# Kernel optimization log

Measured on AMD Instinct MI355X. Metric: run time of the kernel, lower is better.

The kernel has to match this reference:

```python
import jax, jax.numpy as jnp
import numpy as np


def _sqdist(X1, X2):
    # squared euclidean distance matrix, matches torch.cdist(...,p=2)**2
    d2 = (jnp.sum(X1 * X1, -1)[:, None] + jnp.sum(X2 * X2, -1)[None, :]
          - 2.0 * (X1 @ X2.T))
    return jnp.maximum(d2, 0.0)


def setup_inputs() -> dict:
    key = jax.random.key(0)
    k1, k2, k3, k4, k5, k6 = jax.random.split(key, 6)
    n, m, d, C = 1024, 2048, 4, 64
    X_train = jax.random.normal(k1, (n, d), dtype=jnp.float32)
    y_train = jax.random.normal(k2, (n,), dtype=jnp.float32)
    X_test = jax.random.normal(k3, (m, d), dtype=jnp.float32)
    # positive params within the priors' supports
    lengthscale = jax.random.uniform(k4, (C,), minval=0.1, maxval=3.0, dtype=jnp.float32)
    variance = jax.random.uniform(k5, (C,), minval=0.1, maxval=3.0, dtype=jnp.float32)
    noise = jax.random.uniform(k6, (C,), minval=0.01, maxval=0.5, dtype=jnp.float32)
    return {"X_train": X_train, "y_train": y_train, "X_test": X_test,
            "lengthscale": lengthscale, "variance": variance, "noise": noise}


def reference(X_train, y_train, X_test, lengthscale, variance, noise):
    n = X_train.shape[0]
    ls2 = (lengthscale ** 2)[:, None, None]          # [C,1,1]
    var = variance[:, None, None]                     # [C,1,1]
    d2_tr = _sqdist(X_train, X_train)                 # [n,n]
    d2_te = _sqdist(X_test, X_train)                  # [m,n]
    K_train = var * jnp.exp(-0.5 * d2_tr[None] / ls2)   # [C,n,n]
    K_test = var * jnp.exp(-0.5 * d2_te[None] / ls2)    # [C,m,n]
    K_noisy = K_train + noise[:, None, None] * jnp.eye(n, dtype=K_train.dtype)
    L = jnp.linalg.cholesky(K_noisy)                  # batched [C,n,n]

    def per_chain(Lc, Ktc):
        solve = jax.scipy.linalg.solve_triangular
        z = solve(Lc, y_train, lower=True)            # [n]
        alpha = solve(Lc, z, lower=True, trans=1)     # [n]
        pred_mean = Ktc @ alpha                       # [m]
        v = solve(Lc, Ktc.T, lower=True)              # [n,m]
        pred_var = jnp.sum(v * v, axis=0)             # [m]
        return pred_mean, pred_var

    means, vars_ = jax.vmap(per_chain)(L, K_test)     # [C,m] each
    return means.mean(axis=0), vars_.mean(axis=0)
```

## Files before the change

### kernel.cpp

```cpp
#include <hip/hip_runtime.h>
#include <hip/hip_fp16.h>
#include <math.h>

#define N 1024
#define M 2048
#define C 64
#define NB 128
#define TB 8
#define NBLK 36
#define PL ((size_t)NBLK*NB*NB)

typedef __attribute__((ext_vector_type(8))) short bf16x8;
typedef __attribute__((ext_vector_type(8))) _Float16 f16x8;
typedef __attribute__((ext_vector_type(4))) float f32x4;

__device__ __forceinline__ size_t pblk(int ib, int jt){
    return ((size_t)((ib*(ib+1))/2 + jt))*((size_t)NB*NB);
}

#define TT(r,c) T[(r)][(((c)+(r)) & 127)]


__device__ __forceinline__ float sqdist4(const float4 a, const float4 b){
    float dx=a.x-b.x, dy=a.y-b.y, dz=a.z-b.z, dw=a.w-b.w;
    return dx*dx+dy*dy+dz*dz+dw*dw;
}

__device__ __forceinline__ void split4(float x0, float x1, float x2, float x3,
                                       uint2& hi, uint2& lo){
    unsigned b0=__float_as_uint(x0), b1=__float_as_uint(x1),
             b2=__float_as_uint(x2), b3=__float_as_uint(x3);
    unsigned h0=b0&0xFFFF0000u, h1=b1&0xFFFF0000u, h2=b2&0xFFFF0000u, h3=b3&0xFFFF0000u;
    hi.x = (h0>>16)|h1;  hi.y = (h2>>16)|h3;
    float l0=x0-__uint_as_float(h0), l1=x1-__uint_as_float(h1),
          l2=x2-__uint_as_float(h2), l3=x3-__uint_as_float(h3);
    lo.x = (__float_as_uint(l0)>>16) | (__float_as_uint(l1)&0xFFFF0000u);
    lo.y = (__float_as_uint(l2)>>16) | (__float_as_uint(l3)&0xFFFF0000u);
}

__device__ void chol_invert_lds(float T[NB][NB], int tid){
    for (int j = 0; j < NB; j++){
        float d = TT(j,j);
        float inv = 1.0f / sqrtf(d);
        for (int i = j+1+tid; i < NB; i += 256) TT(i,j) *= inv;
        if (tid == 0) TT(j,j) = d * inv;
        __syncthreads();
        int i = j+1 + (tid >> 1);
        if (i < NB){
            float lij = TT(i,j);
            for (int k = j+1+(tid&1); k <= i; k += 2)
                TT(i,k) -= lij * TT(k,j);
        }
        __syncthreads();
    }
    for (int i = 0; i < NB; i++){
        float inv_ii = 1.0f / TT(i,i);
        int j = tid & 127, hi = tid >> 7;
        float S = 0.0f;
        if (j < i){
            for (int k = i-1-hi; k >= j; k -= 2)
                S += TT(i,k) * TT(k,j);
        }
        if (hi && j < i) TT(j,i) = S;
        __syncthreads();
        if (!hi){
            if (j < i)      TT(i,j) = -inv_ii * (S + TT(j,i));
            else if (j == i) TT(i,i) = inv_ii;
        }
        __syncthreads();
    }
}


struct FragLds { __half Ah[4096], Al[4096], Bh[4096], Bl[4096]; };

__device__ __forceinline__ void stage_f16(__half* __restrict__ Hh, __half* __restrict__ Hl,
                                          const float* __restrict__ S, int ld,
                                          int k0, bool contig, int tid){
    #pragma unroll
    for (int h = 0; h < 2; h++){
        int u = tid + h*256;
        int fr = u & 15, kg = (u>>4)&3, rt = (u>>6)&3, hf = u>>8;
        int rc = hf*64 + rt*16 + fr;
        int kk = k0 + kg*8;
        float x[8];
        if (contig){
            float4 v0 = *(const float4*)&S[(size_t)rc*ld + kk];
            float4 v1 = *(const float4*)&S[(size_t)rc*ld + kk + 4];
            x[0]=v0.x;x[1]=v0.y;x[2]=v0.z;x[3]=v0.w;
            x[4]=v1.x;x[5]=v1.y;x[6]=v1.z;x[7]=v1.w;
        } else {
            #pragma unroll
            for (int e=0;e<8;e++) x[e] = S[(size_t)(kk+e)*ld + rc];
        }
        union { __half h[8]; uint4 u4; } Hi, Lo;
        #pragma unroll
        for (int e=0;e<8;e++){
            __half hv = __float2half_rn(x[e]);
            Hi.h[e] = hv;
            Lo.h[e] = __float2half_rn(x[e] - __half2float(hv));
        }
        *(uint4*)&Hh[(size_t)u*8] = Hi.u4;
        *(uint4*)&Hl[(size_t)u*8] = Lo.u4;
    }
}

__device__ __forceinline__ void mfma_slab_f16(const __half* Ah, const __half* Al,
                                              const __half* Bh, const __half* Bl,
                                              int wrow, int wcol, int lane,
                                              f32x4 acc[4][4]){
    f16x8 ah[4], al[4];
    #pragma unroll
    for (int rt=0;rt<4;rt++){
        ah[rt] = *(const f16x8*)&Ah[((size_t)((wrow*4+rt)*64 + lane))*8];
        al[rt] = *(const f16x8*)&Al[((size_t)((wrow*4+rt)*64 + lane))*8];
    }
    #pragma unroll
    for (int ct=0;ct<4;ct++){
        f16x8 bh = *(const f16x8*)&Bh[((size_t)((wcol*4+ct)*64 + lane))*8];
        f16x8 bl = *(const f16x8*)&Bl[((size_t)((wcol*4+ct)*64 + lane))*8];
        #pragma unroll
        for (int rt=0;rt<4;rt++){
            f32x4 a = acc[rt][ct];
            a = __builtin_amdgcn_mfma_f32_16x16x32_f16(ah[rt], bh, a, 0,0,0);
            a = __builtin_amdgcn_mfma_f32_16x16x32_f16(ah[rt], bl, a, 0,0,0);
            a = __builtin_amdgcn_mfma_f32_16x16x32_f16(al[rt], bh, a, 0,0,0);
            acc[rt][ct] = a;
        }
    }
}

__device__ void gemm_f16_unit(const float* __restrict__ A, int lda,
                              const float* __restrict__ B, int ldb, bool bContig,
                              FragLds& F, f32x4 acc[4][4], int tid){
    int lane = tid & 63, w = tid >> 6, wrow = w>>1, wcol = w&1;
    for (int k0 = 0; k0 < NB; k0 += 32){
        __syncthreads();
        stage_f16(F.Ah, F.Al, A, lda, k0, true, tid);
        stage_f16(F.Bh, F.Bl, B, ldb, k0, bContig, tid);
        __syncthreads();
        mfma_slab_f16(F.Ah, F.Al, F.Bh, F.Bl, wrow, wcol, lane, acc);
    }
}

__device__ __forceinline__ void store_f16acc(float* __restrict__ Cp, int ldc,
                                             const f32x4 acc[4][4], float sgn, int tid){
    int lane = tid&63, w = tid>>6, wrow = w>>1, wcol = w&1;
    int fr = lane&15, kg = lane>>4;
    #pragma unroll
    for (int rt=0;rt<4;rt++)
      #pragma unroll
      for (int ct=0;ct<4;ct++)
        #pragma unroll
        for (int r=0;r<4;r++){
            int row = wrow*64 + rt*16 + kg*4 + r;
            int col = wcol*64 + ct*16 + fr;
            Cp[(size_t)row*ldc + col] = sgn*acc[rt][ct][r];
        }
}

#define ZERO_ACC(acc) { _Pragma("unroll") for (int zi=0;zi<4;zi++) _Pragma("unroll") for (int zj=0;zj<4;zj++) acc[zi][zj] = (f32x4)0.0f; }


__global__ void k_init_acc(float* __restrict__ acc){
    int i = blockIdx.x*blockDim.x + threadIdx.x;
    if (i < 2*M) acc[i] = 0.0f;
}

__global__ void k_build_d2te(const float* __restrict__ Xtr, const float* __restrict__ Xte,
                             float* __restrict__ d2){
    int j = blockIdx.x;
    float4 xj = ((const float4*)Xte)[j];
    for (int i = threadIdx.x; i < N; i += blockDim.x){
        float4 xi = ((const float4*)Xtr)[i];
        d2[(size_t)j*N + i] = sqdist4(xi,xj);
    }
}

__global__ __launch_bounds__(256) void k_build_K(const float* __restrict__ Xtr,
                          const float* __restrict__ ls,
                          const float* __restrict__ var, const float* __restrict__ noise,
                          float* __restrict__ Lbuf){
    __shared__ float4 xr[NB], xc[NB];
    int c = blockIdx.y, flat = blockIdx.x;
    int ib = 0; while ((ib+1)*(ib+2)/2 <= flat) ib++;
    int jt = flat - ib*(ib+1)/2;
    int tid = threadIdx.x;
    if (tid < NB) xr[tid] = ((const float4*)Xtr)[ib*NB + tid];
    else          xc[tid-NB] = ((const float4*)Xtr)[jt*NB + (tid-NB)];
    __syncthreads();
    float il2 = 1.0f/(ls[c]*ls[c]);
    float vc = var[c], nc = noise[c];
    float* blk = Lbuf + c*PL + pblk(ib,jt);
    for (int idx = tid; idx < NB*NB; idx += 256){
        int r = idx >> 7, col = idx & 127;
        float d2v = sqdist4(xr[r], xc[col]);
        float v = vc*__expf(-0.5f*d2v*il2);
        if (ib==jt && r==col) v += nc;
        blk[idx] = v;
    }
}

__global__ __launch_bounds__(256) void k_diagF(float* __restrict__ Lbuf){
    __shared__ float T[NB][NB];
    int c = blockIdx.x, tid = threadIdx.x;
    float* A = Lbuf + c*PL + pblk(0,0);
    for (int idx = tid; idx < NB*NB; idx += 256){
        int r = idx >> 7, col = idx & 127;
        TT(r,col) = A[idx];
    }
    __syncthreads();
    chol_invert_lds(T, tid);
    for (int idx = tid; idx < NB*NB; idx += 256){
        int r = idx >> 7, col = idx & 127;
        A[idx] = (col <= r) ? TT(r,col) : 0.0f;
    }
}

__global__ __launch_bounds__(256) void k_panel(float* __restrict__ Lbuf, int kb){
    __shared__ FragLds F;
    int c = blockIdx.x;
    int ib = kb + 1 + blockIdx.y;
    int tid = threadIdx.x;
    float* base = Lbuf + c*PL;
    float* Ablk = base + pblk(ib,kb);
    const float* Dv = base + pblk(kb,kb);
    f32x4 acc[4][4]; ZERO_ACC(acc);
    gemm_f16_unit(Ablk, NB, Dv, NB, true, F, acc, tid);
    store_f16acc(Ablk, NB, acc, 1.0f, tid);
}

union SmU2 { FragLds f; float T[NB][NB]; };
__global__ __launch_bounds__(256) void k_syrk(float* __restrict__ Lbuf, int kb){
    __shared__ SmU2 sm;
    int c = blockIdx.x;
    int flat = blockIdx.y;
    int di = 0; while ((di+1)*(di+2)/2 <= flat) di++;
    int dj = flat - di*(di+1)/2;
    int i = kb+1+di, j = kb+1+dj;
    int tid = threadIdx.x;
    float* base = Lbuf + c*PL;
    float* Cblk = base + pblk(i,j);
    const float* Ablk = base + pblk(i,kb);
    const float* Bblk = base + pblk(j,kb);
    f32x4 acc[4][4]; ZERO_ACC(acc);
    gemm_f16_unit(Ablk, NB, Bblk, NB, true, sm.f, acc, tid);
    int lane = tid&63, w = tid>>6, wrow = w>>1, wcol = w&1;
    int fr = lane&15, kg = lane>>4;
    if (flat != 0){
        #pragma unroll
        for (int rt=0;rt<4;rt++)
          #pragma unroll
          for (int ct=0;ct<4;ct++)
            #pragma unroll
            for (int r=0;r<4;r++){
                int row = wrow*64 + rt*16 + kg*4 + r;
                int col = wcol*64 + ct*16 + fr;
                Cblk[(size_t)row*NB + col] -= acc[rt][ct][r];
            }
    } else {
        __syncthreads();
        float (*T)[NB] = sm.T;
        #pragma unroll
        for (int rt=0;rt<4;rt++)
          #pragma unroll
          for (int ct=0;ct<4;ct++)
            #pragma unroll
            for (int r=0;r<4;r++){
                int row = wrow*64 + rt*16 + kg*4 + r;
                int col = wcol*64 + ct*16 + fr;
                TT(row,col) = Cblk[(size_t)row*NB + col] - acc[rt][ct][r];
            }
        __syncthreads();
        chol_invert_lds(T, tid);
        for (int idx = tid; idx < NB*NB; idx += 256){
            int r = idx >> 7, col = idx & 127;
            Cblk[idx] = (col <= r) ? TT(r,col) : 0.0f;
        }
    }
}

__global__ __launch_bounds__(256) void k_gemmA(float* __restrict__ Trow,
                                               const float* __restrict__ Lbuf, int ib){
    __shared__ FragLds F;
    int c = blockIdx.x, ct = blockIdx.y;
    int tid = threadIdx.x;
    const float* base = Lbuf + c*PL;
    const float* Dv = base + pblk(ib,ib);
    const float* Bsrc = base + pblk(ib,ct);
    f32x4 acc[4][4]; ZERO_ACC(acc);
    gemm_f16_unit(Dv, NB, Bsrc, NB, false, F, acc, tid);
    store_f16acc(Trow + (size_t)c*NB*N + ct*NB, N, acc, 1.0f, tid);
}

__global__ __launch_bounds__(256) void k_gemmB(float* __restrict__ Lbuf,
                                               const float* __restrict__ Trow, int ib){
    __shared__ FragLds F;
    int c = blockIdx.x, jt = blockIdx.y;
    int tid = threadIdx.x;
    const float* G = Trow + (size_t)c*NB*N;
    float* base = Lbuf + c*PL;
    f32x4 acc[4][4]; ZERO_ACC(acc);
    for (int kt = jt; kt < ib; kt++)
        gemm_f16_unit(G + kt*NB, N, base + pblk(kt,jt), NB, false, F, acc, tid);
    store_f16acc(base + pblk(ib,jt), NB, acc, -1.0f, tid);
}

__global__ void k_zvec(const float* __restrict__ Lbuf, const float* __restrict__ y,
                       float* __restrict__ z){
    int c = blockIdx.x;
    int p = blockIdx.y * 4 + (threadIdx.x >> 6);
    int lane = threadIdx.x & 63;
    int pb = p >> 7, pl = p & 127;
    const float* base = Lbuf + c*PL;
    float s = 0.0f;
    for (int kt = 0; kt <= pb; kt++){
        const float* row = base + pblk(pb,kt) + (size_t)pl*NB;
        int lim = (kt==pb) ? pl : NB-1;
        for (int i = lane; i <= lim; i += 64) s += row[i]*y[kt*NB + i];
    }
    for (int off = 32; off; off >>= 1) s += __shfl_down(s, off);
    if (lane == 0) z[c*N + p] = s;
}

__global__ __launch_bounds__(256) void k_wsplit(float* __restrict__ Lbuf){
    int c = blockIdx.y, flat = blockIdx.x;
    int tid = threadIdx.x;
    float* blk = Lbuf + c*PL + (size_t)flat*NB*NB;
    float4 v[16];
    #pragma unroll
    for (int h = 0; h < 8; h++){
        int g = tid + h*256;
        int u = g & 511, slab = g >> 9;
        int fr = u&15, kg = (u>>4)&3, rt = (u>>6)&3, hf = u>>8;
        int row = hf*64 + rt*16 + fr;
        int k = slab*32 + kg*8;
        v[2*h]   = *(const float4*)&blk[(size_t)row*NB + k];
        v[2*h+1] = *(const float4*)&blk[(size_t)row*NB + k + 4];
    }
    __syncthreads();
    unsigned short* out = (unsigned short*)blk;
    #pragma unroll
    for (int h = 0; h < 8; h++){
        int g = tid + h*256;
        int u = g & 511, slab = g >> 9;
        uint2 h0, l0, h1, l1;
        split4(v[2*h].x, v[2*h].y, v[2*h].z, v[2*h].w, h0, l0);
        split4(v[2*h+1].x, v[2*h+1].y, v[2*h+1].z, v[2*h+1].w, h1, l1);
        *(uint4*)&out[((size_t)(slab*2+0)*512 + u)*8] = make_uint4(h0.x,h0.y,h1.x,h1.y);
        *(uint4*)&out[((size_t)(slab*2+1)*512 + u)*8] = make_uint4(l0.x,l0.y,l1.x,l1.y);
    }
}

__global__ __launch_bounds__(256) void k_bigg(const float* __restrict__ Lbuf,
                                              const float* __restrict__ d2,
                                              const float* __restrict__ zbuf,
                                              const float* __restrict__ ls,
                                              const float* __restrict__ var,
                                              float* __restrict__ acc_out){
    __shared__ unsigned short Ah[4096], Al[4096], Bh[4096], Bl[4096];
    int jt = blockIdx.x, pt = blockIdx.y, c = blockIdx.z;
    int tid = threadIdx.x;
    int lane = tid & 63, w = tid >> 6;
    int wrow = w >> 1, wcol = w & 1;
    float il2 = 1.0f/(ls[c]*ls[c]);
    float vc = var[c];
    float ec = -0.5f*il2;
    const float* Arow = d2 + (size_t)(jt*NB)*N;
    const float* Wbase = Lbuf + c*PL;
    int klen = (pt+1)*NB;
    f32x4 acc[4][4]; ZERO_ACC(acc);

    int fr = lane & 15, kg = lane >> 4;
    int q = tid & 7, rs = tid >> 3;
    int kgq = q >> 1, e4 = (q & 1) * 4;

    for (int k0 = 0; k0 < klen; k0 += 32){
        const unsigned short* Wimg = (const unsigned short*)(Wbase + pblk(pt, k0 >> 7));
        int slab = (k0 & 127) >> 5;
        const unsigned short* hi_img = Wimg + (size_t)(slab*2+0)*4096;
        const unsigned short* lo_img = Wimg + (size_t)(slab*2+1)*4096;
        __syncthreads();
        #pragma unroll
        for (int p = 0; p < 4; p++){
            int row = rs + 32*p;
            float4 dv = *(const float4*)&Arow[(size_t)row*N + k0 + q*4];
            float x0 = vc*__expf(ec*dv.x), x1 = vc*__expf(ec*dv.y);
            float x2 = vc*__expf(ec*dv.z), x3 = vc*__expf(ec*dv.w);
            uint2 hi, lo; split4(x0,x1,x2,x3, hi, lo);
            int u = (row&15) + kgq*16 + ((row>>4)&3)*64 + (row>>6)*256;
            *(uint2*)&Ah[(size_t)u*8 + e4] = hi;
            *(uint2*)&Al[(size_t)u*8 + e4] = lo;
        }
        #pragma unroll
        for (int h2 = 0; h2 < 2; h2++){
            int u = tid + h2*256;
            *(uint4*)&Bh[(size_t)u*8] = *(const uint4*)&hi_img[(size_t)u*8];
            *(uint4*)&Bl[(size_t)u*8] = *(const uint4*)&lo_img[(size_t)u*8];
        }
        __syncthreads();
        bf16x8 ah[4], al[4];
        #pragma unroll
        for (int rt=0;rt<4;rt++){
            ah[rt] = *(const bf16x8*)&Ah[((size_t)((wrow*4+rt)*64 + lane))*8];
            al[rt] = *(const bf16x8*)&Al[((size_t)((wrow*4+rt)*64 + lane))*8];
        }
        #pragma unroll
        for (int ct=0;ct<4;ct++){
            bf16x8 bh = *(const bf16x8*)&Bh[((size_t)((wcol*4+ct)*64 + lane))*8];
            bf16x8 bl = *(const bf16x8*)&Bl[((size_t)((wcol*4+ct)*64 + lane))*8];
            #pragma unroll
            for (int rt=0;rt<4;rt++){
                f32x4 a = acc[rt][ct];
                a = __builtin_amdgcn_mfma_f32_16x16x32_bf16(ah[rt], bh, a, 0,0,0);
                a = __builtin_amdgcn_mfma_f32_16x16x32_bf16(ah[rt], bl, a, 0,0,0);
                a = __builtin_amdgcn_mfma_f32_16x16x32_bf16(al[rt], bh, a, 0,0,0);
                acc[rt][ct] = a;
            }
        }
    }
    float zv[4];
    #pragma unroll
    for (int ct=0;ct<4;ct++) zv[ct] = zbuf[c*N + pt*NB + wcol*64 + ct*16 + fr];
    #pragma unroll
    for (int rt=0;rt<4;rt++){
        #pragma unroll
        for (int r=0;r<4;r++){
            float m = 0.0f, v = 0.0f;
            #pragma unroll
            for (int ct=0;ct<4;ct++){
                float x = acc[rt][ct][r];
                v += x*x; m += x*zv[ct];
            }
            m += __shfl_xor(m, 1);  v += __shfl_xor(v, 1);
            m += __shfl_xor(m, 2);  v += __shfl_xor(v, 2);
            m += __shfl_xor(m, 4);  v += __shfl_xor(v, 4);
            m += __shfl_xor(m, 8);  v += __shfl_xor(v, 8);
            if (fr == 0){
                int j = jt*NB + wrow*64 + rt*16 + kg*4 + r;
                atomicAdd(&acc_out[j], m);
                atomicAdd(&acc_out[M + j], v);
            }
        }
    }
}

__global__ void k_final(const float* __restrict__ acc, float* __restrict__ out){
    int i = blockIdx.x*blockDim.x + threadIdx.x;
    if (i < 2*M) out[i] = acc[i] * (1.0f/64.0f);
}


extern "C" void kernel_launch(void* const* d_in, const int* in_sizes, int n_in,
                              void* d_out, int out_size, void* d_ws, size_t ws_size,
                              hipStream_t stream) {
    const float* Xtr = (const float*)d_in[0];
    const float* ytr = (const float*)d_in[1];
    const float* Xte = (const float*)d_in[2];
    const float* ls  = (const float*)d_in[3];
    const float* var = (const float*)d_in[4];
    const float* noi = (const float*)d_in[5];
    float* out = (float*)d_out;

    float* ws = (float*)d_ws;
    const size_t shared_fl  = (size_t)N*M + 2*M;
    const size_t perchain   = PL + (size_t)NB*N + (size_t)N;
    size_t avail = ws_size / sizeof(float);
    if (avail < shared_fl + perchain) return;
    int Gmax = (int)((avail - shared_fl) / perchain);
    if (Gmax > C) Gmax = C;
    int nbatch = (C + Gmax - 1) / Gmax;
    int G = (C + nbatch - 1) / nbatch;

    float* d2te = ws;
    float* acc  = d2te + (size_t)N*M;
    float* Lbuf = acc  + 2*M;
    float* Trow = Lbuf + (size_t)G*PL;
    float* zbuf = Trow + (size_t)G*NB*N;

    k_init_acc<<<dim3((2*M+255)/256), dim3(256), 0, stream>>>(acc);
    k_build_d2te<<<dim3(M), dim3(256), 0, stream>>>(Xtr, Xte, d2te);

    for (int c0 = 0; c0 < C; c0 += G){
        int g = C - c0 < G ? C - c0 : G;

        k_build_K<<<dim3(NBLK, g), dim3(256), 0, stream>>>(Xtr, ls+c0, var+c0, noi+c0, Lbuf);
        k_diagF<<<dim3(g), dim3(256), 0, stream>>>(Lbuf);

        for (int kb = 0; kb < TB-1; kb++){
            int rem = TB-1-kb;
            k_panel<<<dim3(g, rem), dim3(256), 0, stream>>>(Lbuf, kb);
            k_syrk<<<dim3(g, rem*(rem+1)/2), dim3(256), 0, stream>>>(Lbuf, kb);
        }
        for (int ib = 1; ib < TB; ib++){
            k_gemmA<<<dim3(g, ib), dim3(256), 0, stream>>>(Trow, Lbuf, ib);
            k_gemmB<<<dim3(g, ib), dim3(256), 0, stream>>>(Lbuf, Trow, ib);
        }
        k_zvec<<<dim3(g, N/4), dim3(256), 0, stream>>>(Lbuf, ytr, zbuf);
        k_wsplit<<<dim3(NBLK, g), dim3(256), 0, stream>>>(Lbuf);
        k_bigg<<<dim3(M/NB, TB, g), dim3(256), 0, stream>>>(Lbuf, d2te, zbuf, ls+c0, var+c0, acc);
    }
    k_final<<<dim3((2*M+255)/256), dim3(256), 0, stream>>>(acc, out);
}
```

Measured before the change: 5.532 ms.

## Pair panel tiles in bigg kernel, fuse diagonal factor into build_K

The big GEMM kernel now handles two panel tiles per block (pt0, pt1), so the exp-computed K_test A-tile is built once and used by both accumulators. This halves the grid's redundant exp/split work. The variance scale moves out of the exp loop into the epilogue (vc and vc^2). The first diagonal-block Cholesky inversion is folded into the flat==0 block of k_build_K, which removes one launch. In exchange the kernel carries twice the accumulator registers and more LDS, which may lower occupancy, and the work per block is uneven because pt1 needs a longer k range.

```diff
diff --git a/kernel.cpp b/kernel.cpp
--- a/kernel.cpp
+++ b/kernel.cpp
@@ -73,6 +73,8 @@
 
 
 struct FragLds { __half Ah[4096], Al[4096], Bh[4096], Bl[4096]; };
+struct SmX { float4 xr[NB]; float4 xc[NB]; };
+union SmU { FragLds f; float T[NB][NB]; SmX x; };
 
 __device__ __forceinline__ void stage_f16(__half* __restrict__ Hh, __half* __restrict__ Hl,
                                           const float* __restrict__ S, int ld,
@@ -177,43 +179,47 @@
     }
 }
 
+__global__ void k_final(const float* __restrict__ acc, float* __restrict__ out){
+    int i = blockIdx.x*blockDim.x + threadIdx.x;
+    if (i < 2*M) out[i] = acc[i] * (1.0f/64.0f);
+}
+
 __global__ __launch_bounds__(256) void k_build_K(const float* __restrict__ Xtr,
                           const float* __restrict__ ls,
                           const float* __restrict__ var, const float* __restrict__ noise,
                           float* __restrict__ Lbuf){
-    __shared__ float4 xr[NB], xc[NB];
+    __shared__ SmU sm;
     int c = blockIdx.y, flat = blockIdx.x;
     int ib = 0; while ((ib+1)*(ib+2)/2 <= flat) ib++;
     int jt = flat - ib*(ib+1)/2;
     int tid = threadIdx.x;
-    if (tid < NB) xr[tid] = ((const float4*)Xtr)[ib*NB + tid];
-    else          xc[tid-NB] = ((const float4*)Xtr)[jt*NB + (tid-NB)];
+    if (tid < NB) sm.x.xr[tid] = ((const float4*)Xtr)[ib*NB + tid];
+    else          sm.x.xc[tid-NB] = ((const float4*)Xtr)[jt*NB + (tid-NB)];
     __syncthreads();
     float il2 = 1.0f/(ls[c]*ls[c]);
     float vc = var[c], nc = noise[c];
     float* blk = Lbuf + c*PL + pblk(ib,jt);
     for (int idx = tid; idx < NB*NB; idx += 256){
         int r = idx >> 7, col = idx & 127;
-        float d2v = sqdist4(xr[r], xc[col]);
+        float d2v = sqdist4(sm.x.xr[r], sm.x.xc[col]);
         float v = vc*__expf(-0.5f*d2v*il2);
         if (ib==jt && r==col) v += nc;
         blk[idx] = v;
     }
-}
-
-__global__ __launch_bounds__(256) void k_diagF(float* __restrict__ Lbuf){
-    __shared__ float T[NB][NB];
-    int c = blockIdx.x, tid = threadIdx.x;
-    float* A = Lbuf + c*PL + pblk(0,0);
-    for (int idx = tid; idx < NB*NB; idx += 256){
-        int r = idx >> 7, col = idx & 127;
-        TT(r,col) = A[idx];
-    }
-    __syncthreads();
-    chol_invert_lds(T, tid);
-    for (int idx = tid; idx < NB*NB; idx += 256){
-        int r = idx >> 7, col = idx & 127;
-        A[idx] = (col <= r) ? TT(r,col) : 0.0f;
+    if (flat == 0){
+        __threadfence_block();
+        __syncthreads();
+        float (*T)[NB] = sm.T;
+        for (int idx = tid; idx < NB*NB; idx += 256){
+            int r = idx >> 7, col = idx & 127;
+            TT(r,col) = blk[idx];
+        }
+        __syncthreads();
+        chol_invert_lds(T, tid);
+        for (int idx = tid; idx < NB*NB; idx += 256){
+            int r = idx >> 7, col = idx & 127;
+            blk[idx] = (col <= r) ? TT(r,col) : 0.0f;
+        }
     }
 }
 
@@ -222,7 +228,7 @@
     int c = blockIdx.x;
     int ib = kb + 1 + blockIdx.y;
     int tid = threadIdx.x;
-    float* base = Lbuf + c*PL;
+    float* base = Lbuf + (size_t)c*PL;
     float* Ablk = base + pblk(ib,kb);
     const float* Dv = base + pblk(kb,kb);
     f32x4 acc[4][4]; ZERO_ACC(acc);
@@ -230,16 +236,15 @@
     store_f16acc(Ablk, NB, acc, 1.0f, tid);
 }
 
-union SmU2 { FragLds f; float T[NB][NB]; };
 __global__ __launch_bounds__(256) void k_syrk(float* __restrict__ Lbuf, int kb){
-    __shared__ SmU2 sm;
+    __shared__ SmU sm;
     int c = blockIdx.x;
     int flat = blockIdx.y;
     int di = 0; while ((di+1)*(di+2)/2 <= flat) di++;
     int dj = flat - di*(di+1)/2;
     int i = kb+1+di, j = kb+1+dj;
     int tid = threadIdx.x;
-    float* base = Lbuf + c*PL;
+    float* base = Lbuf + (size_t)c*PL;
     float* Cblk = base + pblk(i,j);
     const float* Ablk = base + pblk(i,kb);
     const float* Bblk = base + pblk(j,kb);
@@ -285,7 +290,7 @@
     __shared__ FragLds F;
     int c = blockIdx.x, ct = blockIdx.y;
     int tid = threadIdx.x;
-    const float* base = Lbuf + c*PL;
+    const float* base = Lbuf + (size_t)c*PL;
     const float* Dv = base + pblk(ib,ib);
     const float* Bsrc = base + pblk(ib,ct);
     f32x4 acc[4][4]; ZERO_ACC(acc);
@@ -299,7 +304,7 @@
     int c = blockIdx.x, jt = blockIdx.y;
     int tid = threadIdx.x;
     const float* G = Trow + (size_t)c*NB*N;
-    float* base = Lbuf + c*PL;
+    float* base = Lbuf + (size_t)c*PL;
     f32x4 acc[4][4]; ZERO_ACC(acc);
     for (int kt = jt; kt < ib; kt++)
         gemm_f16_unit(G + kt*NB, N, base + pblk(kt,jt), NB, false, F, acc, tid);
@@ -312,7 +317,7 @@
     int p = blockIdx.y * 4 + (threadIdx.x >> 6);
     int lane = threadIdx.x & 63;
     int pb = p >> 7, pl = p & 127;
-    const float* base = Lbuf + c*PL;
+    const float* base = Lbuf + (size_t)c*PL;
     float s = 0.0f;
     for (int kt = 0; kt <= pb; kt++){
         const float* row = base + pblk(pb,kt) + (size_t)pl*NB;
@@ -358,8 +363,11 @@
                                               const float* __restrict__ ls,
                                               const float* __restrict__ var,
                                               float* __restrict__ acc_out){
-    __shared__ unsigned short Ah[4096], Al[4096], Bh[4096], Bl[4096];
-    int jt = blockIdx.x, pt = blockIdx.y, c = blockIdx.z;
+    __shared__ unsigned short Ah[4096], Al[4096];
+    __shared__ unsigned short B0h[4096], B0l[4096];
+    __shared__ unsigned short B1h[4096], B1l[4096];
+    int jt = blockIdx.x, pp = blockIdx.y, c = blockIdx.z;
+    int pt0 = pp*2, pt1 = pt0+1;
     int tid = threadIdx.x;
     int lane = tid & 63, w = tid >> 6;
     int wrow = w >> 1, wcol = w & 1;
@@ -367,26 +375,28 @@
     float vc = var[c];
     float ec = -0.5f*il2;
     const float* Arow = d2 + (size_t)(jt*NB)*N;
-    const float* Wbase = Lbuf + c*PL;
-    int klen = (pt+1)*NB;
-    f32x4 acc[4][4]; ZERO_ACC(acc);
+    const float* Wbase = Lbuf + (size_t)c*PL;
+    int klen0 = (pt0+1)*NB, klen1 = (pt1+1)*NB;
+    f32x4 acc0[4][4]; ZERO_ACC(acc0);
+    f32x4 acc1[4][4]; ZERO_ACC(acc1);
 
     int fr = lane & 15, kg = lane >> 4;
     int q = tid & 7, rs = tid >> 3;
     int kgq = q >> 1, e4 = (q & 1) * 4;
 
-    for (int k0 = 0; k0 < klen; k0 += 32){
-        const unsigned short* Wimg = (const unsigned short*)(Wbase + pblk(pt, k0 >> 7));
+    for (int k0 = 0; k0 < klen1; k0 += 32){
         int slab = (k0 & 127) >> 5;
-        const unsigned short* hi_img = Wimg + (size_t)(slab*2+0)*4096;
-        const unsigned short* lo_img = Wimg + (size_t)(slab*2+1)*4096;
+        const unsigned short* i1h = (const unsigned short*)(Wbase + pblk(pt1, k0 >> 7))
+                                    + (size_t)(slab*2)*4096;
+        const unsigned short* i1l = i1h + 4096;
+        bool act0 = (k0 < klen0);
         __syncthreads();
         #pragma unroll
         for (int p = 0; p < 4; p++){
             int row = rs + 32*p;
             float4 dv = *(const float4*)&Arow[(size_t)row*N + k0 + q*4];
-            float x0 = vc*__expf(ec*dv.x), x1 = vc*__expf(ec*dv.y);
-            float x2 = vc*__expf(ec*dv.z), x3 = vc*__expf(ec*dv.w);
+            float x0 = __expf(ec*dv.x), x1 = __expf(ec*dv.y);
+            float x2 = __expf(ec*dv.z), x3 = __expf(ec*dv.w);
             uint2 hi, lo; split4(x0,x1,x2,x3, hi, lo);
             int u = (row&15) + kgq*16 + ((row>>4)&3)*64 + (row>>6)*256;
             *(uint2*)&Ah[(size_t)u*8 + e4] = hi;
@@ -395,8 +405,19 @@
         #pragma unroll
         for (int h2 = 0; h2 < 2; h2++){
             int u = tid + h2*256;
-            *(uint4*)&Bh[(size_t)u*8] = *(const uint4*)&hi_img[(size_t)u*8];
-            *(uint4*)&Bl[(size_t)u*8] = *(const uint4*)&lo_img[(size_t)u*8];
+            *(uint4*)&B1h[(size_t)u*8] = *(const uint4*)&i1h[(size_t)u*8];
+            *(uint4*)&B1l[(size_t)u*8] = *(const uint4*)&i1l[(size_t)u*8];
+        }
+        if (act0){
+            const unsigned short* i0h = (const unsigned short*)(Wbase + pblk(pt0, k0 >> 7))
+                                        + (size_t)(slab*2)*4096;
+            const unsigned short* i0l = i0h + 4096;
+            #pragma unroll
+            for (int h2 = 0; h2 < 2; h2++){
+                int u = tid + h2*256;
+                *(uint4*)&B0h[(size_t)u*8] = *(const uint4*)&i0h[(size_t)u*8];
+                *(uint4*)&B0l[(size_t)u*8] = *(const uint4*)&i0l[(size_t)u*8];
+            }
         }
         __syncthreads();
         bf16x8 ah[4], al[4];
@@ -407,47 +428,63 @@
         }
         #pragma unroll
         for (int ct=0;ct<4;ct++){
-            bf16x8 bh = *(const bf16x8*)&Bh[((size_t)((wcol*4+ct)*64 + lane))*8];
-            bf16x8 bl = *(const bf16x8*)&Bl[((size_t)((wcol*4+ct)*64 + lane))*8];
+            bf16x8 bh = *(const bf16x8*)&B1h[((size_t)((wcol*4+ct)*64 + lane))*8];
+            bf16x8 bl = *(const bf16x8*)&B1l[((size_t)((wcol*4+ct)*64 + lane))*8];
             #pragma unroll
             for (int rt=0;rt<4;rt++){
-                f32x4 a = acc[rt][ct];
+                f32x4 a = acc1[rt][ct];
                 a = __builtin_amdgcn_mfma_f32_16x16x32_bf16(ah[rt], bh, a, 0,0,0);
                 a = __builtin_amdgcn_mfma_f32_16x16x32_bf16(ah[rt], bl, a, 0,0,0);
                 a = __builtin_amdgcn_mfma_f32_16x16x32_bf16(al[rt], bh, a, 0,0,0);
-                acc[rt][ct] = a;
+                acc1[rt][ct] = a;
             }
         }
-    }
-    float zv[4];
-    #pragma unroll
-    for (int ct=0;ct<4;ct++) zv[ct] = zbuf[c*N + pt*NB + wcol*64 + ct*16 + fr];
-    #pragma unroll
-    for (int rt=0;rt<4;rt++){
-        #pragma unroll
-        for (int r=0;r<4;r++){
-            float m = 0.0f, v = 0.0f;
+        if (act0){
             #pragma unroll
             for (int ct=0;ct<4;ct++){
-                float x = acc[rt][ct][r];
-                v += x*x; m += x*zv[ct];
+                bf16x8 bh = *(const bf16x8*)&B0h[((size_t)((wcol*4+ct)*64 + lane))*8];
+                bf16x8 bl = *(const bf16x8*)&B0l[((size_t)((wcol*4+ct)*64 + lane))*8];
+                #pragma unroll
+                for (int rt=0;rt<4;rt++){
+                    f32x4 a = acc0[rt][ct];
+                    a = __builtin_amdgcn_mfma_f32_16x16x32_bf16(ah[rt], bh, a, 0,0,0);
+                    a = __builtin_amdgcn_mfma_f32_16x16x32_bf16(ah[rt], bl, a, 0,0,0);
+                    a = __builtin_amdgcn_mfma_f32_16x16x32_bf16(al[rt], bh, a, 0,0,0);
+                    acc0[rt][ct] = a;
+                }
             }
-            m += __shfl_xor(m, 1);  v += __shfl_xor(v, 1);
-            m += __shfl_xor(m, 2);  v += __shfl_xor(v, 2);
-            m += __shfl_xor(m, 4);  v += __shfl_xor(v, 4);
-            m += __shfl_xor(m, 8);  v += __shfl_xor(v, 8);
-            if (fr == 0){
-                int j = jt*NB + wrow*64 + rt*16 + kg*4 + r;
-                atomicAdd(&acc_out[j], m);
-                atomicAdd(&acc_out[M + j], v);
-            }
-        }
-    }
-}
-
-__global__ void k_final(const float* __restrict__ acc, float* __restrict__ out){
-    int i = blockIdx.x*blockDim.x + threadIdx.x;
-    if (i < 2*M) out[i] = acc[i] * (1.0f/64.0f);
+        }
+    }
+    float vc2 = vc*vc;
+    #define EPILOGUE(ACC, PT) {                                                   \
+        float zv[4];                                                              \
+        _Pragma("unroll")                                                         \
+        for (int ct=0;ct<4;ct++) zv[ct] = zbuf[c*N + (PT)*NB + wcol*64 + ct*16 + fr]; \
+        _Pragma("unroll")                                                         \
+        for (int rt=0;rt<4;rt++){                                                 \
+            _Pragma("unroll")                                                     \
+            for (int r=0;r<4;r++){                                                \
+                float m = 0.0f, v = 0.0f;                                         \
+                _Pragma("unroll")                                                 \
+                for (int ct=0;ct<4;ct++){                                         \
+                    float x = ACC[rt][ct][r];                                     \
+                    v += x*x; m += x*zv[ct];                                      \
+                }                                                                 \
+                m += __shfl_xor(m, 1);  v += __shfl_xor(v, 1);                    \
+                m += __shfl_xor(m, 2);  v += __shfl_xor(v, 2);                    \
+                m += __shfl_xor(m, 4);  v += __shfl_xor(v, 4);                    \
+                m += __shfl_xor(m, 8);  v += __shfl_xor(v, 8);                    \
+                if (fr == 0){                                                     \
+                    int j = jt*NB + wrow*64 + rt*16 + kg*4 + r;                   \
+                    atomicAdd(&acc_out[j], vc*m);                                 \
+                    atomicAdd(&acc_out[M + j], vc2*v);                            \
+                }                                                                 \
+            }                                                                     \
+        }                                                                         \
+    }
+    EPILOGUE(acc0, pt0)
+    EPILOGUE(acc1, pt1)
+    #undef EPILOGUE
 }
 
 
@@ -485,7 +522,6 @@
         int g = C - c0 < G ? C - c0 : G;
 
         k_build_K<<<dim3(NBLK, g), dim3(256), 0, stream>>>(Xtr, ls+c0, var+c0, noi+c0, Lbuf);
-        k_diagF<<<dim3(g), dim3(256), 0, stream>>>(Lbuf);
 
         for (int kb = 0; kb < TB-1; kb++){
             int rem = TB-1-kb;
@@ -498,7 +534,7 @@
         }
         k_zvec<<<dim3(g, N/4), dim3(256), 0, stream>>>(Lbuf, ytr, zbuf);
         k_wsplit<<<dim3(NBLK, g), dim3(256), 0, stream>>>(Lbuf);
-        k_bigg<<<dim3(M/NB, TB, g), dim3(256), 0, stream>>>(Lbuf, d2te, zbuf, ls+c0, var+c0, acc);
+        k_bigg<<<dim3(M/NB, TB/2, g), dim3(256), 0, stream>>>(Lbuf, d2te, zbuf, ls+c0, var+c0, acc);
     }
     k_final<<<dim3((2*M+255)/256), dim3(256), 0, stream>>>(acc, out);
 }
```

Result: slower. 5.817 ms (+5.2%).
